# Performance work log

Measured on AMD Instinct MI355X. Metric: run time of the kernel, lower is better.

## Reference

```python
import jax, jax.numpy as jnp
import numpy as np

HIDDEN = 1024
HEADS = 16
HEAD_DIM = HIDDEN // HEADS

def setup_inputs() -> dict:
    key = jax.random.key(0)
    ks = jax.random.split(key, 11)
    B, T, D = 2, 2048, HIDDEN
    s = 1.0 / np.sqrt(D)
    return {
        "query": jax.random.normal(ks[0], (B, T, D), jnp.float32),
        "key": jax.random.normal(ks[1], (B, T, D), jnp.float32),
        "value": jax.random.normal(ks[2], (B, T, D), jnp.float32),
        "Wq": jax.random.normal(ks[3], (D, D), jnp.float32) * s,
        "bq": jnp.zeros((D,), jnp.float32),
        "Wk": jax.random.normal(ks[4], (D, D), jnp.float32) * s,
        "bk": jnp.zeros((D,), jnp.float32),
        "Wv": jax.random.normal(ks[5], (D, D), jnp.float32) * s,
        "bv": jnp.zeros((D,), jnp.float32),
        "Wo": jax.random.normal(ks[6], (D, D), jnp.float32) * s,
        "bo": jnp.zeros((D,), jnp.float32),
    }

def reference(query, key, value, Wq, bq, Wk, bk, Wv, bv, Wo, bo):
    B, Tq, D = query.shape
    Tk = key.shape[1]
    H, Hd = HEADS, HEAD_DIM
    # projections -> [B, H, T, Hd]
    Q = (query @ Wq + bq).reshape(B, Tq, H, Hd).transpose(0, 2, 1, 3)
    K = (key @ Wk + bk).reshape(B, Tk, H, Hd).transpose(0, 2, 1, 3)
    V = (value @ Wv + bv).reshape(B, Tk, H, Hd).transpose(0, 2, 1, 3)
    scale = jnp.sqrt(jnp.asarray(Hd, Q.dtype))
    scores = jnp.einsum('bhqd,bhkd->bhqk', Q, K) / scale  # [B,H,Tq,Tk]
    causal = jnp.triu(jnp.ones((Tq, Tk), bool), k=1)
    scores = jnp.where(causal[None, None], jnp.asarray(-jnp.inf, scores.dtype), scores)
    attn = jax.nn.softmax(scores, axis=-1)
    out = jnp.einsum('bhqk,bhkd->bhqd', attn, V)  # [B,H,Tq,Hd]
    out = out.transpose(0, 2, 1, 3).reshape(B, Tq, D)
    return out @ Wo + bo
```

## Files before the change

kernel.cpp:

```cpp
#include <hip/hip_runtime.h>
#include <hip/hip_bf16.h>


typedef __bf16 bf16_t;
typedef __bf16 bf16x8 __attribute__((ext_vector_type(8)));
typedef float f32x4 __attribute__((ext_vector_type(4)));
typedef unsigned int u32;

#define D_MODEL 1024
#define SEQ_T   2048
#define NHEAD   16
#define HDIM    64
#define M_ROWS  4096
#define MEGA    (1024 * 1024)

__device__ __forceinline__ void gl2lds16(const void* g, void* l) {
    __builtin_amdgcn_global_load_lds((const __attribute__((address_space(1))) u32*)g,
                                     (__attribute__((address_space(3))) u32*)l, 16, 0, 0);
}

__global__ __launch_bounds__(256) void prep(
    const float* __restrict__ Wq, const float* __restrict__ Wk,
    const float* __restrict__ Wv, const float* __restrict__ Wo,
    const float* __restrict__ Xq, const float* __restrict__ Xk, const float* __restrict__ Xv,
    bf16_t* __restrict__ Wqt, bf16_t* __restrict__ Wkt,
    bf16_t* __restrict__ Wvt, bf16_t* __restrict__ Wot,
    bf16_t* __restrict__ Xb)
{
    int blk = blockIdx.x, tid = threadIdx.x;
    if (blk < 4096) {
        int wi = blk >> 10, t = blk & 1023;
        int n0 = (t & 31) * 32, k0 = (t >> 5) * 32;
        const float* W = wi == 0 ? Wq : (wi == 1 ? Wk : (wi == 2 ? Wv : Wo));
        bf16_t* Wt = wi == 0 ? Wqt : (wi == 1 ? Wkt : (wi == 2 ? Wvt : Wot));
        __shared__ float tile[32][33];
        int tx = tid & 31, ty = tid >> 5;
#pragma unroll
        for (int i = 0; i < 32; i += 8)
            tile[ty + i][tx] = W[(k0 + ty + i) * D_MODEL + n0 + tx];
        __syncthreads();
#pragma unroll
        for (int i = 0; i < 32; i += 8)
            Wt[(size_t)(n0 + ty + i) * D_MODEL + k0 + tx] = (bf16_t)tile[tx][ty + i];
    } else {
        int b2 = blk - 4096;
        int xi = b2 >> 10;
        const float* X = xi == 0 ? Xq : (xi == 1 ? Xk : Xv);
        bf16_t* XB = Xb + (size_t)xi * M_ROWS * D_MODEL;
        size_t base = (size_t)(b2 & 1023) * 4096 + tid * 16;
        const float4* xp = (const float4*)(X + base);
        float4 a0 = xp[0], a1 = xp[1], a2 = xp[2], a3 = xp[3];
        bf16x8 o0, o1;
        o0[0] = (bf16_t)a0.x; o0[1] = (bf16_t)a0.y; o0[2] = (bf16_t)a0.z; o0[3] = (bf16_t)a0.w;
        o0[4] = (bf16_t)a1.x; o0[5] = (bf16_t)a1.y; o0[6] = (bf16_t)a1.z; o0[7] = (bf16_t)a1.w;
        o1[0] = (bf16_t)a2.x; o1[1] = (bf16_t)a2.y; o1[2] = (bf16_t)a2.z; o1[3] = (bf16_t)a2.w;
        o1[4] = (bf16_t)a3.x; o1[5] = (bf16_t)a3.y; o1[6] = (bf16_t)a3.z; o1[7] = (bf16_t)a3.w;
        *(bf16x8*)(XB + base) = o0;
        *(bf16x8*)(XB + base + 8) = o1;
    }
}

template <bool PRECAST>
__global__ __launch_bounds__(256) void proj_fused(
    const float* __restrict__ Xq, const float* __restrict__ Xk, const float* __restrict__ Xv,
    const bf16_t* __restrict__ Xb,
    const bf16_t* __restrict__ Wqt, const bf16_t* __restrict__ Wkt, const bf16_t* __restrict__ Wvt,
    const float* __restrict__ bq, const float* __restrict__ bk, const float* __restrict__ bv,
    bf16_t* __restrict__ Qh, bf16_t* __restrict__ Kh, bf16_t* __restrict__ Vt)
{
    __shared__ bf16_t Ab[128 * 32];
    __shared__ bf16_t Bb[128 * 32];
    int tid = threadIdx.x;
    int w = tid >> 6, lane = tid & 63, lo16 = lane & 15, quad = lane >> 4;
    int m0 = blockIdx.x * 128;
    int proj = blockIdx.y >> 3;
    int n0 = (blockIdx.y & 7) * 128;
    const float*  X    = proj == 0 ? Xq  : (proj == 1 ? Xk  : Xv);
    const bf16_t* XB   = Xb + (size_t)proj * M_ROWS * D_MODEL;
    const bf16_t* Wt   = proj == 0 ? Wqt : (proj == 1 ? Wkt : Wvt);
    const float*  bias = proj == 0 ? bq  : (proj == 1 ? bk  : bv);
    int wm = (w >> 1) * 64, wn = (w & 1) * 64;

    f32x4 acc[4][4];
#pragma unroll
    for (int i = 0; i < 4; i++)
#pragma unroll
        for (int j = 0; j < 4; j++) acc[i][j] = (f32x4){0.f, 0.f, 0.f, 0.f};

    for (int k0 = 0; k0 < D_MODEL; k0 += 32) {
        __syncthreads();
#pragma unroll
        for (int p = 0; p < 2; p++) {
            int idx = p * 256 + tid;
            int row = idx >> 2, ch = (idx & 3) * 8;
            if (PRECAST) {
                gl2lds16(XB + (size_t)(m0 + row) * D_MODEL + k0 + ch, Ab + idx * 8);
            } else {
                const float* as = X + (size_t)(m0 + row) * D_MODEL + k0 + ch;
                float4 a0 = *(const float4*)as, a1 = *(const float4*)(as + 4);
                bf16x8 av;
                av[0] = (bf16_t)a0.x; av[1] = (bf16_t)a0.y; av[2] = (bf16_t)a0.z; av[3] = (bf16_t)a0.w;
                av[4] = (bf16_t)a1.x; av[5] = (bf16_t)a1.y; av[6] = (bf16_t)a1.z; av[7] = (bf16_t)a1.w;
                *(bf16x8*)(Ab + idx * 8) = av;
            }
            gl2lds16(Wt + (size_t)(n0 + row) * D_MODEL + k0 + ch, Bb + idx * 8);
        }
        __syncthreads();
        bf16x8 af[4], bfr[4];
#pragma unroll
        for (int i = 0; i < 4; i++)
            af[i] = *(bf16x8*)(Ab + (wm + i * 16 + lo16) * 32 + quad * 8);
#pragma unroll
        for (int j = 0; j < 4; j++)
            bfr[j] = *(bf16x8*)(Bb + (wn + j * 16 + lo16) * 32 + quad * 8);
#pragma unroll
        for (int i = 0; i < 4; i++)
#pragma unroll
            for (int j = 0; j < 4; j++)
                acc[i][j] = __builtin_amdgcn_mfma_f32_16x16x32_bf16(af[i], bfr[j], acc[i][j], 0, 0, 0);
    }

    float qscale = proj == 0 ? 0.125f : 1.0f;
#pragma unroll
    for (int j = 0; j < 4; j++) {
        int col = n0 + wn + j * 16 + lo16;
        float bv2 = bias[col];
        int h = col >> 6, hd = col & 63;
#pragma unroll
        for (int i = 0; i < 4; i++) {
#pragma unroll
            for (int r = 0; r < 4; r++) {
                int m = m0 + wm + i * 16 + quad * 4 + r;
                int b = m >> 11, t = m & 2047;
                bf16_t val = (bf16_t)((acc[i][j][r] + bv2) * qscale);
                if (proj == 2)
                    Vt[(((size_t)(b * NHEAD + h) * HDIM + hd) * SEQ_T) + t] = val;
                else if (proj == 1)
                    Kh[(((size_t)(b * NHEAD + h) * SEQ_T + t) * HDIM) + hd] = val;
                else
                    Qh[(((size_t)(b * NHEAD + h) * SEQ_T + t) * HDIM) + hd] = val;
            }
        }
    }
}

__global__ __launch_bounds__(128, 2) void flash_attn(const bf16_t* __restrict__ Qh,
                                                     const bf16_t* __restrict__ Kh,
                                                     const bf16_t* __restrict__ Vt,
                                                     bf16_t* __restrict__ Ob) {
    int bh = blockIdx.x & 31;
    int qt = 31 - (int)(blockIdx.x >> 5);
    int tid = threadIdx.x;
    int w = tid >> 6, lane = tid & 63, lo16 = lane & 15, quad = lane >> 4;
    int qbase = qt * 64 + w * 32;

    __shared__ bf16_t KL[64 * 64];
    __shared__ bf16_t VL[64 * 64];
    __shared__ bf16_t PL[2][32 * 64];
    bf16_t* myP = PL[w];

    const bf16_t* Qp = Qh + (size_t)bh * SEQ_T * HDIM;
    const bf16_t* Kp = Kh + (size_t)bh * SEQ_T * HDIM;
    const bf16_t* Vp = Vt + (size_t)bh * HDIM * SEQ_T;

    bf16x8 qf[2][2];
#pragma unroll
    for (int m = 0; m < 2; m++) {
        const bf16_t* qr = Qp + (size_t)(qbase + m * 16 + lo16) * HDIM;
        qf[m][0] = *(const bf16x8*)(qr + quad * 8);
        qf[m][1] = *(const bf16x8*)(qr + 32 + quad * 8);
    }

    bf16x8 ones;
#pragma unroll
    for (int i = 0; i < 8; i++) ones[i] = (bf16_t)1.0f;

    f32x4 oacc[2][4], lacc[2];
#pragma unroll
    for (int m = 0; m < 2; m++) {
        lacc[m] = (f32x4){0.f, 0.f, 0.f, 0.f};
#pragma unroll
        for (int s = 0; s < 4; s++) oacc[m][s] = (f32x4){0.f, 0.f, 0.f, 0.f};
    }

    int nkt = qt + 1;
    for (int kt = 0; kt < nkt; kt++) {
        __syncthreads();
#pragma unroll
        for (int p = 0; p < 4; p++) {
            int idx = p * 128 + tid;
            int row = idx >> 3, cp = idx & 7, cl = (cp - row) & 7;
            gl2lds16(Kp + (size_t)(kt * 64 + row) * HDIM + cl * 8, (bf16_t*)KL + idx * 8);
            gl2lds16(Vp + (size_t)row * SEQ_T + kt * 64 + cl * 8, (bf16_t*)VL + idx * 8);
        }
        __syncthreads();

        f32x4 sacc[2][4];
#pragma unroll
        for (int m = 0; m < 2; m++)
#pragma unroll
            for (int s = 0; s < 4; s++) sacc[m][s] = (f32x4){0.f, 0.f, 0.f, 0.f};
#pragma unroll
        for (int s = 0; s < 4; s++) {
            int keyl = s * 16 + lo16;
            bf16x8 kf0 = *(bf16x8*)(KL + keyl * 64 + ((quad + keyl) & 7) * 8);
            bf16x8 kf1 = *(bf16x8*)(KL + keyl * 64 + ((quad + 4 + keyl) & 7) * 8);
#pragma unroll
            for (int m = 0; m < 2; m++) {
                sacc[m][s] = __builtin_amdgcn_mfma_f32_16x16x32_bf16(qf[m][0], kf0, sacc[m][s], 0, 0, 0);
                sacc[m][s] = __builtin_amdgcn_mfma_f32_16x16x32_bf16(qf[m][1], kf1, sacc[m][s], 0, 0, 0);
            }
        }

        bool diag = (kt == qt);
        bf16x8 pf[2][2];
#pragma unroll
        for (int m = 0; m < 2; m++) {
#pragma unroll
            for (int s = 0; s < 4; s++) {
                int col = s * 16 + lo16;
#pragma unroll
                for (int r = 0; r < 4; r++) {
                    int rowl = m * 16 + quad * 4 + r;
                    float p = __expf(sacc[m][s][r]);
                    if (diag) {
                        int key = kt * 64 + col, qq = qbase + rowl;
                        p = (key <= qq) ? p : 0.f;
                    }
                    int phys = ((col >> 3) + rowl + (rowl >> 3)) & 7;
                    myP[rowl * 64 + phys * 8 + (col & 7)] = (bf16_t)p;
                }
            }
            int rowA = m * 16 + lo16;
            int Rr = (rowA + (rowA >> 3)) & 7;
            pf[m][0] = *(bf16x8*)(myP + rowA * 64 + ((quad + Rr) & 7) * 8);
            pf[m][1] = *(bf16x8*)(myP + rowA * 64 + ((quad + 4 + Rr) & 7) * 8);
            lacc[m] = __builtin_amdgcn_mfma_f32_16x16x32_bf16(pf[m][0], ones, lacc[m], 0, 0, 0);
            lacc[m] = __builtin_amdgcn_mfma_f32_16x16x32_bf16(pf[m][1], ones, lacc[m], 0, 0, 0);
        }

#pragma unroll
        for (int s = 0; s < 4; s++) {
            int dl = s * 16 + lo16;
            bf16x8 vf0 = *(bf16x8*)(VL + dl * 64 + ((quad + dl) & 7) * 8);
            bf16x8 vf1 = *(bf16x8*)(VL + dl * 64 + ((quad + 4 + dl) & 7) * 8);
#pragma unroll
            for (int m = 0; m < 2; m++) {
                oacc[m][s] = __builtin_amdgcn_mfma_f32_16x16x32_bf16(pf[m][0], vf0, oacc[m][s], 0, 0, 0);
                oacc[m][s] = __builtin_amdgcn_mfma_f32_16x16x32_bf16(pf[m][1], vf1, oacc[m][s], 0, 0, 0);
            }
        }
    }

    int b = bh >> 4, h = bh & 15;
#pragma unroll
    for (int m = 0; m < 2; m++)
#pragma unroll
        for (int s = 0; s < 4; s++) {
            int d = s * 16 + lo16;
#pragma unroll
            for (int r = 0; r < 4; r++) {
                int q = qbase + m * 16 + quad * 4 + r;
                float o = oacc[m][s][r] / lacc[m][r];
                Ob[((size_t)b * SEQ_T + q) * D_MODEL + h * HDIM + d] = (bf16_t)o;
            }
        }
}

__global__ __launch_bounds__(256) void out_gemm(const bf16_t* __restrict__ A,
                                                const bf16_t* __restrict__ Wt,
                                                const float* __restrict__ bias,
                                                float* __restrict__ out) {
    __shared__ bf16_t Ab[128 * 32];
    __shared__ bf16_t Bb[128 * 32];
    int tid = threadIdx.x;
    int w = tid >> 6, lane = tid & 63, lo16 = lane & 15, quad = lane >> 4;
    int m0 = blockIdx.x * 128;
    int n0 = blockIdx.y * 128;
    int wm = (w >> 1) * 64, wn = (w & 1) * 64;

    f32x4 acc[4][4];
#pragma unroll
    for (int i = 0; i < 4; i++)
#pragma unroll
        for (int j = 0; j < 4; j++) acc[i][j] = (f32x4){0.f, 0.f, 0.f, 0.f};

    for (int k0 = 0; k0 < D_MODEL; k0 += 32) {
        __syncthreads();
#pragma unroll
        for (int p = 0; p < 2; p++) {
            int idx = p * 256 + tid;
            int row = idx >> 2, ch = (idx & 3) * 8;
            gl2lds16(A  + (size_t)(m0 + row) * D_MODEL + k0 + ch, Ab + idx * 8);
            gl2lds16(Wt + (size_t)(n0 + row) * D_MODEL + k0 + ch, Bb + idx * 8);
        }
        __syncthreads();
        bf16x8 af[4], bfr[4];
#pragma unroll
        for (int i = 0; i < 4; i++)
            af[i] = *(bf16x8*)(Ab + (wm + i * 16 + lo16) * 32 + quad * 8);
#pragma unroll
        for (int j = 0; j < 4; j++)
            bfr[j] = *(bf16x8*)(Bb + (wn + j * 16 + lo16) * 32 + quad * 8);
#pragma unroll
        for (int i = 0; i < 4; i++)
#pragma unroll
            for (int j = 0; j < 4; j++)
                acc[i][j] = __builtin_amdgcn_mfma_f32_16x16x32_bf16(af[i], bfr[j], acc[i][j], 0, 0, 0);
    }

#pragma unroll
    for (int j = 0; j < 4; j++) {
        int col = n0 + wn + j * 16 + lo16;
        float bv2 = bias[col];
#pragma unroll
        for (int i = 0; i < 4; i++)
#pragma unroll
            for (int r = 0; r < 4; r++) {
                int m = m0 + wm + i * 16 + quad * 4 + r;
                out[(size_t)m * D_MODEL + col] = acc[i][j][r] + bv2;
            }
    }
}

extern "C" void kernel_launch(void* const* d_in, const int* in_sizes, int n_in,
                              void* d_out, int out_size, void* d_ws, size_t ws_size,
                              hipStream_t stream) {
    const float* q  = (const float*)d_in[0];
    const float* k  = (const float*)d_in[1];
    const float* v  = (const float*)d_in[2];
    const float* Wq = (const float*)d_in[3];
    const float* bq = (const float*)d_in[4];
    const float* Wk = (const float*)d_in[5];
    const float* bk = (const float*)d_in[6];
    const float* Wv = (const float*)d_in[7];
    const float* bv = (const float*)d_in[8];
    const float* Wo = (const float*)d_in[9];
    const float* bo = (const float*)d_in[10];
    float* out = (float*)d_out;

    bf16_t* Wqt = (bf16_t*)d_ws;
    bf16_t* Wkt = Wqt + (size_t)MEGA;
    bf16_t* Wvt = Wkt + (size_t)MEGA;
    bf16_t* Wot = Wvt + (size_t)MEGA;
    bf16_t* Qh  = Wot + (size_t)MEGA;
    bf16_t* Kh  = Qh  + (size_t)M_ROWS * D_MODEL;
    bf16_t* Vt  = Kh  + (size_t)M_ROWS * D_MODEL;
    bf16_t* Xb  = Vt  + (size_t)M_ROWS * D_MODEL;
    bf16_t* Ob  = Xb;

    bool precast = ws_size >= (size_t)(4 * MEGA + 3 * M_ROWS * D_MODEL + 3 * M_ROWS * D_MODEL) * sizeof(bf16_t);

    int prep_blocks = precast ? 4096 + 3 * 1024 : 4096;
    prep<<<prep_blocks, 256, 0, stream>>>(Wq, Wk, Wv, Wo, q, k, v, Wqt, Wkt, Wvt, Wot, Xb);

    dim3 pg(M_ROWS / 128, 24);
    if (precast)
        proj_fused<true><<<pg, 256, 0, stream>>>(q, k, v, Xb, Wqt, Wkt, Wvt, bq, bk, bv, Qh, Kh, Vt);
    else
        proj_fused<false><<<pg, 256, 0, stream>>>(q, k, v, Xb, Wqt, Wkt, Wvt, bq, bk, bv, Qh, Kh, Vt);

    flash_attn<<<32 * 32, 128, 0, stream>>>(Qh, Kh, Vt, Ob);

    dim3 og(M_ROWS / 128, D_MODEL / 128);
    out_gemm<<<og, 256, 0, stream>>>(Ob, Wot, bo, out);
}
```

Before: 229.1 us.

## Rework attention to keep P in registers, pair causal tiles, widen GEMM K-tiles

The flash attention kernel now computes S transposed (K as the A operand), so the exponentiated probabilities land directly in the register layout that 16x16x16 MFMA needs for the PV product. This removes the per-wave P staging in LDS and the ones-vector MFMA used for row sums, which are replaced by scalar accumulation and a cross-lane shuffle. Each block now handles a long and a short causal query tile to balance work, using half as many blocks. The projection and output GEMMs move to 64-wide K tiles with swizzled LDS, and the output GEMM uses 128x64 tiles; this trades more LDS per block and more blocks for fewer barriers.

Result: slower. 236.8 us (+3.3%).

```diff
diff --git a/kernel.cpp b/kernel.cpp
--- a/kernel.cpp
+++ b/kernel.cpp
@@ -4,6 +4,9 @@
 
 typedef __bf16 bf16_t;
 typedef __bf16 bf16x8 __attribute__((ext_vector_type(8)));
+typedef __bf16 bf16x4 __attribute__((ext_vector_type(4)));
+typedef __bf16 bf16x2 __attribute__((ext_vector_type(2)));
+typedef short short4v __attribute__((ext_vector_type(4)));
 typedef float f32x4 __attribute__((ext_vector_type(4)));
 typedef unsigned int u32;
 
@@ -17,6 +20,10 @@
 __device__ __forceinline__ void gl2lds16(const void* g, void* l) {
     __builtin_amdgcn_global_load_lds((const __attribute__((address_space(1))) u32*)g,
                                      (__attribute__((address_space(3))) u32*)l, 16, 0, 0);
+}
+
+__device__ __forceinline__ short4v as_s4(bf16x4 v) {
+    union { bf16x4 h; short4v s; } u; u.h = v; return u.s;
 }
 
 __global__ __launch_bounds__(256) void prep(
@@ -68,8 +75,8 @@
     const float* __restrict__ bq, const float* __restrict__ bk, const float* __restrict__ bv,
     bf16_t* __restrict__ Qh, bf16_t* __restrict__ Kh, bf16_t* __restrict__ Vt)
 {
-    __shared__ bf16_t Ab[128 * 32];
-    __shared__ bf16_t Bb[128 * 32];
+    __shared__ bf16_t Ab[128 * 64];
+    __shared__ bf16_t Bb[128 * 64];
     int tid = threadIdx.x;
     int w = tid >> 6, lane = tid & 63, lo16 = lane & 15, quad = lane >> 4;
     int m0 = blockIdx.x * 128;
@@ -87,37 +94,44 @@
 #pragma unroll
         for (int j = 0; j < 4; j++) acc[i][j] = (f32x4){0.f, 0.f, 0.f, 0.f};
 
-    for (int k0 = 0; k0 < D_MODEL; k0 += 32) {
-        __syncthreads();
-#pragma unroll
-        for (int p = 0; p < 2; p++) {
+    for (int k0 = 0; k0 < D_MODEL; k0 += 64) {
+        __syncthreads();
+#pragma unroll
+        for (int p = 0; p < 4; p++) {
             int idx = p * 256 + tid;
-            int row = idx >> 2, ch = (idx & 3) * 8;
+            int row = idx >> 3, cp = idx & 7, cl = (cp - row) & 7;
             if (PRECAST) {
-                gl2lds16(XB + (size_t)(m0 + row) * D_MODEL + k0 + ch, Ab + idx * 8);
+                gl2lds16(XB + (size_t)(m0 + row) * D_MODEL + k0 + cl * 8, Ab + idx * 8);
             } else {
-                const float* as = X + (size_t)(m0 + row) * D_MODEL + k0 + ch;
+                const float* as = X + (size_t)(m0 + row) * D_MODEL + k0 + cl * 8;
                 float4 a0 = *(const float4*)as, a1 = *(const float4*)(as + 4);
                 bf16x8 av;
                 av[0] = (bf16_t)a0.x; av[1] = (bf16_t)a0.y; av[2] = (bf16_t)a0.z; av[3] = (bf16_t)a0.w;
                 av[4] = (bf16_t)a1.x; av[5] = (bf16_t)a1.y; av[6] = (bf16_t)a1.z; av[7] = (bf16_t)a1.w;
                 *(bf16x8*)(Ab + idx * 8) = av;
             }
-            gl2lds16(Wt + (size_t)(n0 + row) * D_MODEL + k0 + ch, Bb + idx * 8);
-        }
-        __syncthreads();
-        bf16x8 af[4], bfr[4];
-#pragma unroll
-        for (int i = 0; i < 4; i++)
-            af[i] = *(bf16x8*)(Ab + (wm + i * 16 + lo16) * 32 + quad * 8);
-#pragma unroll
-        for (int j = 0; j < 4; j++)
-            bfr[j] = *(bf16x8*)(Bb + (wn + j * 16 + lo16) * 32 + quad * 8);
-#pragma unroll
-        for (int i = 0; i < 4; i++)
-#pragma unroll
-            for (int j = 0; j < 4; j++)
-                acc[i][j] = __builtin_amdgcn_mfma_f32_16x16x32_bf16(af[i], bfr[j], acc[i][j], 0, 0, 0);
+            gl2lds16(Wt + (size_t)(n0 + row) * D_MODEL + k0 + cl * 8, Bb + idx * 8);
+        }
+        __syncthreads();
+#pragma unroll
+        for (int kh = 0; kh < 2; kh++) {
+            bf16x8 af[4], bfr[4];
+#pragma unroll
+            for (int i = 0; i < 4; i++) {
+                int row = wm + i * 16 + lo16;
+                af[i] = *(bf16x8*)(Ab + row * 64 + (((kh * 4 + quad) + row) & 7) * 8);
+            }
+#pragma unroll
+            for (int j = 0; j < 4; j++) {
+                int row = wn + j * 16 + lo16;
+                bfr[j] = *(bf16x8*)(Bb + row * 64 + (((kh * 4 + quad) + row) & 7) * 8);
+            }
+#pragma unroll
+            for (int i = 0; i < 4; i++)
+#pragma unroll
+                for (int j = 0; j < 4; j++)
+                    acc[i][j] = __builtin_amdgcn_mfma_f32_16x16x32_bf16(af[i], bfr[j], acc[i][j], 0, 0, 0);
+        }
     }
 
     float qscale = proj == 0 ? 0.125f : 1.0f;
@@ -144,173 +158,186 @@
     }
 }
 
-__global__ __launch_bounds__(128, 2) void flash_attn(const bf16_t* __restrict__ Qh,
-                                                     const bf16_t* __restrict__ Kh,
-                                                     const bf16_t* __restrict__ Vt,
-                                                     bf16_t* __restrict__ Ob) {
+__global__ __launch_bounds__(128) void flash_attn(const bf16_t* __restrict__ Qh,
+                                                  const bf16_t* __restrict__ Kh,
+                                                  const bf16_t* __restrict__ Vt,
+                                                  bf16_t* __restrict__ Ob) {
     int bh = blockIdx.x & 31;
-    int qt = 31 - (int)(blockIdx.x >> 5);
+    int pr = blockIdx.x >> 5;
     int tid = threadIdx.x;
     int w = tid >> 6, lane = tid & 63, lo16 = lane & 15, quad = lane >> 4;
-    int qbase = qt * 64 + w * 32;
 
     __shared__ bf16_t KL[64 * 64];
     __shared__ bf16_t VL[64 * 64];
-    __shared__ bf16_t PL[2][32 * 64];
-    bf16_t* myP = PL[w];
 
     const bf16_t* Qp = Qh + (size_t)bh * SEQ_T * HDIM;
     const bf16_t* Kp = Kh + (size_t)bh * SEQ_T * HDIM;
     const bf16_t* Vp = Vt + (size_t)bh * HDIM * SEQ_T;
-
-    bf16x8 qf[2][2];
-#pragma unroll
-    for (int m = 0; m < 2; m++) {
-        const bf16_t* qr = Qp + (size_t)(qbase + m * 16 + lo16) * HDIM;
-        qf[m][0] = *(const bf16x8*)(qr + quad * 8);
-        qf[m][1] = *(const bf16x8*)(qr + 32 + quad * 8);
-    }
-
-    bf16x8 ones;
-#pragma unroll
-    for (int i = 0; i < 8; i++) ones[i] = (bf16_t)1.0f;
-
-    f32x4 oacc[2][4], lacc[2];
-#pragma unroll
-    for (int m = 0; m < 2; m++) {
-        lacc[m] = (f32x4){0.f, 0.f, 0.f, 0.f};
-#pragma unroll
-        for (int s = 0; s < 4; s++) oacc[m][s] = (f32x4){0.f, 0.f, 0.f, 0.f};
-    }
-
-    int nkt = qt + 1;
-    for (int kt = 0; kt < nkt; kt++) {
-        __syncthreads();
-#pragma unroll
-        for (int p = 0; p < 4; p++) {
-            int idx = p * 128 + tid;
-            int row = idx >> 3, cp = idx & 7, cl = (cp - row) & 7;
-            gl2lds16(Kp + (size_t)(kt * 64 + row) * HDIM + cl * 8, (bf16_t*)KL + idx * 8);
-            gl2lds16(Vp + (size_t)row * SEQ_T + kt * 64 + cl * 8, (bf16_t*)VL + idx * 8);
-        }
-        __syncthreads();
-
-        f32x4 sacc[2][4];
-#pragma unroll
-        for (int m = 0; m < 2; m++)
-#pragma unroll
-            for (int s = 0; s < 4; s++) sacc[m][s] = (f32x4){0.f, 0.f, 0.f, 0.f};
-#pragma unroll
-        for (int s = 0; s < 4; s++) {
-            int keyl = s * 16 + lo16;
-            bf16x8 kf0 = *(bf16x8*)(KL + keyl * 64 + ((quad + keyl) & 7) * 8);
-            bf16x8 kf1 = *(bf16x8*)(KL + keyl * 64 + ((quad + 4 + keyl) & 7) * 8);
-#pragma unroll
-            for (int m = 0; m < 2; m++) {
-                sacc[m][s] = __builtin_amdgcn_mfma_f32_16x16x32_bf16(qf[m][0], kf0, sacc[m][s], 0, 0, 0);
-                sacc[m][s] = __builtin_amdgcn_mfma_f32_16x16x32_bf16(qf[m][1], kf1, sacc[m][s], 0, 0, 0);
-            }
-        }
-
-        bool diag = (kt == qt);
-        bf16x8 pf[2][2];
-#pragma unroll
-        for (int m = 0; m < 2; m++) {
+    int b = bh >> 4, h = bh & 15;
+
+#pragma unroll
+    for (int u = 0; u < 2; u++) {
+        int qt = u == 0 ? (31 - pr) : pr;
+        int qbase = qt * 64 + w * 32;
+
+        bf16x8 qf[2][2];
+#pragma unroll
+        for (int n = 0; n < 2; n++) {
+            const bf16_t* qr = Qp + (size_t)(qbase + n * 16 + lo16) * HDIM;
+            qf[n][0] = *(const bf16x8*)(qr + quad * 8);
+            qf[n][1] = *(const bf16x8*)(qr + 32 + quad * 8);
+        }
+
+        f32x4 oacc[2][4];
+        float lsum[2] = {0.f, 0.f};
+#pragma unroll
+        for (int n = 0; n < 2; n++)
+#pragma unroll
+            for (int t = 0; t < 4; t++) oacc[n][t] = (f32x4){0.f, 0.f, 0.f, 0.f};
+
+        for (int kt = 0; kt <= qt; kt++) {
+            __syncthreads();
+#pragma unroll
+            for (int p = 0; p < 4; p++) {
+                int idx = p * 128 + tid;
+                int row = idx >> 3, cp = idx & 7, cl = (cp - row) & 7;
+                gl2lds16(Kp + (size_t)(kt * 64 + row) * HDIM + cl * 8, (bf16_t*)KL + idx * 8);
+                gl2lds16(Vp + (size_t)row * SEQ_T + kt * 64 + cl * 8, (bf16_t*)VL + idx * 8);
+            }
+            __syncthreads();
+
+            bf16x8 kf[4][2];
 #pragma unroll
             for (int s = 0; s < 4; s++) {
-                int col = s * 16 + lo16;
-#pragma unroll
-                for (int r = 0; r < 4; r++) {
-                    int rowl = m * 16 + quad * 4 + r;
-                    float p = __expf(sacc[m][s][r]);
-                    if (diag) {
-                        int key = kt * 64 + col, qq = qbase + rowl;
-                        p = (key <= qq) ? p : 0.f;
+                int keyr = s * 16 + lo16;
+                kf[s][0] = *(bf16x8*)(KL + keyr * 64 + ((quad + keyr) & 7) * 8);
+                kf[s][1] = *(bf16x8*)(KL + keyr * 64 + ((quad + 4 + keyr) & 7) * 8);
+            }
+
+            bool diag = (kt == qt);
+            short4v pf[2][4];
+#pragma unroll
+            for (int n = 0; n < 2; n++) {
+                f32x4 sacc[4];
+#pragma unroll
+                for (int s = 0; s < 4; s++) sacc[s] = (f32x4){0.f, 0.f, 0.f, 0.f};
+#pragma unroll
+                for (int s = 0; s < 4; s++) {
+                    sacc[s] = __builtin_amdgcn_mfma_f32_16x16x32_bf16(kf[s][0], qf[n][0], sacc[s], 0, 0, 0);
+                    sacc[s] = __builtin_amdgcn_mfma_f32_16x16x32_bf16(kf[s][1], qf[n][1], sacc[s], 0, 0, 0);
+                }
+                int q = qbase + n * 16 + lo16;
+#pragma unroll
+                for (int s = 0; s < 4; s++) {
+                    bf16x4 pv;
+#pragma unroll
+                    for (int r = 0; r < 4; r++) {
+                        float e = __expf(sacc[s][r]);
+                        if (diag) {
+                            int key = kt * 64 + s * 16 + quad * 4 + r;
+                            e = (key <= q) ? e : 0.f;
+                        }
+                        lsum[n] += e;
+                        pv[r] = (bf16_t)e;
                     }
-                    int phys = ((col >> 3) + rowl + (rowl >> 3)) & 7;
-                    myP[rowl * 64 + phys * 8 + (col & 7)] = (bf16_t)p;
+                    pf[n][s] = as_s4(pv);
                 }
             }
-            int rowA = m * 16 + lo16;
-            int Rr = (rowA + (rowA >> 3)) & 7;
-            pf[m][0] = *(bf16x8*)(myP + rowA * 64 + ((quad + Rr) & 7) * 8);
-            pf[m][1] = *(bf16x8*)(myP + rowA * 64 + ((quad + 4 + Rr) & 7) * 8);
-            lacc[m] = __builtin_amdgcn_mfma_f32_16x16x32_bf16(pf[m][0], ones, lacc[m], 0, 0, 0);
-            lacc[m] = __builtin_amdgcn_mfma_f32_16x16x32_bf16(pf[m][1], ones, lacc[m], 0, 0, 0);
-        }
-
-#pragma unroll
-        for (int s = 0; s < 4; s++) {
-            int dl = s * 16 + lo16;
-            bf16x8 vf0 = *(bf16x8*)(VL + dl * 64 + ((quad + dl) & 7) * 8);
-            bf16x8 vf1 = *(bf16x8*)(VL + dl * 64 + ((quad + 4 + dl) & 7) * 8);
-#pragma unroll
-            for (int m = 0; m < 2; m++) {
-                oacc[m][s] = __builtin_amdgcn_mfma_f32_16x16x32_bf16(pf[m][0], vf0, oacc[m][s], 0, 0, 0);
-                oacc[m][s] = __builtin_amdgcn_mfma_f32_16x16x32_bf16(pf[m][1], vf1, oacc[m][s], 0, 0, 0);
-            }
-        }
-    }
-
-    int b = bh >> 4, h = bh & 15;
-#pragma unroll
-    for (int m = 0; m < 2; m++)
-#pragma unroll
-        for (int s = 0; s < 4; s++) {
-            int d = s * 16 + lo16;
-#pragma unroll
-            for (int r = 0; r < 4; r++) {
-                int q = qbase + m * 16 + quad * 4 + r;
-                float o = oacc[m][s][r] / lacc[m][r];
-                Ob[((size_t)b * SEQ_T + q) * D_MODEL + h * HDIM + d] = (bf16_t)o;
-            }
-        }
+
+#pragma unroll
+            for (int t = 0; t < 4; t++) {
+                int drow = t * 16 + lo16;
+#pragma unroll
+                for (int s = 0; s < 4; s++) {
+                    int c = s * 16 + quad * 4;
+                    int phys = ((c >> 3) + drow) & 7;
+                    bf16x4 vf = *(bf16x4*)(VL + drow * 64 + phys * 8 + (c & 7));
+                    short4v vfs = as_s4(vf);
+                    oacc[0][t] = __builtin_amdgcn_mfma_f32_16x16x16bf16_1k(vfs, pf[0][s], oacc[0][t], 0, 0, 0);
+                    oacc[1][t] = __builtin_amdgcn_mfma_f32_16x16x16bf16_1k(vfs, pf[1][s], oacc[1][t], 0, 0, 0);
+                }
+            }
+        }
+
+#pragma unroll
+        for (int n = 0; n < 2; n++) {
+            float lt = lsum[n];
+            lt += __shfl_xor(lt, 16);
+            lt += __shfl_xor(lt, 32);
+            float inv = 1.f / lt;
+            int q = qbase + n * 16 + lo16;
+            bf16_t* dst = Ob + ((size_t)b * SEQ_T + q) * D_MODEL + h * HDIM;
+#pragma unroll
+            for (int t = 0; t < 4; t++) {
+#pragma unroll
+                for (int rp = 0; rp < 2; rp++) {
+                    int d0 = t * 16 + quad * 4 + rp * 2;
+                    bf16x2 pk;
+                    pk[0] = (bf16_t)(oacc[n][t][rp * 2] * inv);
+                    pk[1] = (bf16_t)(oacc[n][t][rp * 2 + 1] * inv);
+                    *(bf16x2*)(dst + d0) = pk;
+                }
+            }
+        }
+    }
 }
 
 __global__ __launch_bounds__(256) void out_gemm(const bf16_t* __restrict__ A,
                                                 const bf16_t* __restrict__ Wt,
                                                 const float* __restrict__ bias,
                                                 float* __restrict__ out) {
-    __shared__ bf16_t Ab[128 * 32];
-    __shared__ bf16_t Bb[128 * 32];
+    __shared__ bf16_t Ab[128 * 64];
+    __shared__ bf16_t Bb[64 * 64];
     int tid = threadIdx.x;
     int w = tid >> 6, lane = tid & 63, lo16 = lane & 15, quad = lane >> 4;
     int m0 = blockIdx.x * 128;
-    int n0 = blockIdx.y * 128;
-    int wm = (w >> 1) * 64, wn = (w & 1) * 64;
-
-    f32x4 acc[4][4];
+    int n0 = blockIdx.y * 64;
+    int wm = (w >> 1) * 64, wn = (w & 1) * 32;
+
+    f32x4 acc[4][2];
 #pragma unroll
     for (int i = 0; i < 4; i++)
 #pragma unroll
-        for (int j = 0; j < 4; j++) acc[i][j] = (f32x4){0.f, 0.f, 0.f, 0.f};
-
-    for (int k0 = 0; k0 < D_MODEL; k0 += 32) {
-        __syncthreads();
+        for (int j = 0; j < 2; j++) acc[i][j] = (f32x4){0.f, 0.f, 0.f, 0.f};
+
+    for (int k0 = 0; k0 < D_MODEL; k0 += 64) {
+        __syncthreads();
+#pragma unroll
+        for (int p = 0; p < 4; p++) {
+            int idx = p * 256 + tid;
+            int row = idx >> 3, cp = idx & 7, cl = (cp - row) & 7;
+            gl2lds16(A + (size_t)(m0 + row) * D_MODEL + k0 + cl * 8, Ab + idx * 8);
+        }
 #pragma unroll
         for (int p = 0; p < 2; p++) {
             int idx = p * 256 + tid;
-            int row = idx >> 2, ch = (idx & 3) * 8;
-            gl2lds16(A  + (size_t)(m0 + row) * D_MODEL + k0 + ch, Ab + idx * 8);
-            gl2lds16(Wt + (size_t)(n0 + row) * D_MODEL + k0 + ch, Bb + idx * 8);
-        }
-        __syncthreads();
-        bf16x8 af[4], bfr[4];
-#pragma unroll
-        for (int i = 0; i < 4; i++)
-            af[i] = *(bf16x8*)(Ab + (wm + i * 16 + lo16) * 32 + quad * 8);
-#pragma unroll
-        for (int j = 0; j < 4; j++)
-            bfr[j] = *(bf16x8*)(Bb + (wn + j * 16 + lo16) * 32 + quad * 8);
-#pragma unroll
-        for (int i = 0; i < 4; i++)
-#pragma unroll
-            for (int j = 0; j < 4; j++)
-                acc[i][j] = __builtin_amdgcn_mfma_f32_16x16x32_bf16(af[i], bfr[j], acc[i][j], 0, 0, 0);
-    }
-
-#pragma unroll
-    for (int j = 0; j < 4; j++) {
+            int row = idx >> 3, cp = idx & 7, cl = (cp - row) & 7;
+            gl2lds16(Wt + (size_t)(n0 + row) * D_MODEL + k0 + cl * 8, Bb + idx * 8);
+        }
+        __syncthreads();
+#pragma unroll
+        for (int kh = 0; kh < 2; kh++) {
+            bf16x8 af[4], bfr[2];
+#pragma unroll
+            for (int i = 0; i < 4; i++) {
+                int row = wm + i * 16 + lo16;
+                af[i] = *(bf16x8*)(Ab + row * 64 + (((kh * 4 + quad) + row) & 7) * 8);
+            }
+#pragma unroll
+            for (int j = 0; j < 2; j++) {
+                int row = wn + j * 16 + lo16;
+                bfr[j] = *(bf16x8*)(Bb + row * 64 + (((kh * 4 + quad) + row) & 7) * 8);
+            }
+#pragma unroll
+            for (int i = 0; i < 4; i++)
+#pragma unroll
+                for (int j = 0; j < 2; j++)
+                    acc[i][j] = __builtin_amdgcn_mfma_f32_16x16x32_bf16(af[i], bfr[j], acc[i][j], 0, 0, 0);
+        }
+    }
+
+#pragma unroll
+    for (int j = 0; j < 2; j++) {
         int col = n0 + wn + j * 16 + lo16;
         float bv2 = bias[col];
 #pragma unroll
@@ -349,7 +376,7 @@
     bf16_t* Xb  = Vt  + (size_t)M_ROWS * D_MODEL;
     bf16_t* Ob  = Xb;
 
-    bool precast = ws_size >= (size_t)(4 * MEGA + 3 * M_ROWS * D_MODEL + 3 * M_ROWS * D_MODEL) * sizeof(bf16_t);
+    bool precast = ws_size >= (size_t)(4 * MEGA + 6 * M_ROWS * D_MODEL) * sizeof(bf16_t);
 
     int prep_blocks = precast ? 4096 + 3 * 1024 : 4096;
     prep<<<prep_blocks, 256, 0, stream>>>(Wq, Wk, Wv, Wo, q, k, v, Wqt, Wkt, Wvt, Wot, Xb);
@@ -360,8 +387,8 @@
     else
         proj_fused<false><<<pg, 256, 0, stream>>>(q, k, v, Xb, Wqt, Wkt, Wvt, bq, bk, bv, Qh, Kh, Vt);
 
-    flash_attn<<<32 * 32, 128, 0, stream>>>(Qh, Kh, Vt, Ob);
-
-    dim3 og(M_ROWS / 128, D_MODEL / 128);
+    flash_attn<<<32 * 16, 128, 0, stream>>>(Qh, Kh, Vt, Ob);
+
+    dim3 og(M_ROWS / 128, D_MODEL / 64);
     out_gemm<<<og, 256, 0, stream>>>(Ob, Wot, bo, out);
 }
```
